# Optimization experiments

Hardware: AMD Instinct MI355X
Metric: run time of the kernel (lower is better)

The kernel has to match this reference:

```python
import jax, jax.numpy as jnp
import numpy as np

N, E = 50000, 800000
C, H, EC = 64, 3, 32  # node_channels, heads, edge_channels
NEG_SLOPE = 0.2


def _kaiming(key, shape, fan_in):
    bound = np.sqrt(6.0 / fan_in)  # kaiming_uniform_ default (a=sqrt(5)-ish approx; gain sqrt(2) variant)
    return jax.random.uniform(key, shape, jnp.float32, -bound, bound)


def setup_inputs() -> dict:
    key = jax.random.key(0)
    ks = jax.random.split(key, 8)
    x = jax.random.normal(ks[0], (N, C), jnp.float32)
    edge_index = jax.random.randint(ks[1], (2, E), 0, N, jnp.int64)
    edge_attr = jax.random.normal(ks[2], (E, EC), jnp.float32)
    weight_node = _kaiming(ks[3], (C, H * C), C)
    weight_edge = _kaiming(ks[4], (EC, H * C), EC)
    weight_triplet_att = _kaiming(ks[5], (1, H, 3 * C), 3 * C)
    weight_scale = _kaiming(ks[6], (H * C, C), H * C)
    bias = jnp.zeros((C,), jnp.float32)
    return {"x": x, "edge_index": edge_index, "edge_attr": edge_attr,
            "weight_node": weight_node, "weight_edge": weight_edge,
            "weight_triplet_att": weight_triplet_att,
            "weight_scale": weight_scale, "bias": bias}


def reference(x, edge_index, edge_attr, weight_node, weight_edge,
              weight_triplet_att, weight_scale, bias):
    src = edge_index[0]  # j (source)
    dst = edge_index[1]  # i (target), PyG default flow source_to_target

    xp = x @ weight_node                     # [N, H*C]
    ep = edge_attr @ weight_edge             # [E, H*C]

    x_j = xp[src].reshape(E, H, C)
    x_i = xp[dst].reshape(E, H, C)
    e_ij = ep.reshape(E, H, C)

    # attention weight split along concat order [x_i, e_ij, x_j]
    w = weight_triplet_att.reshape(H, 3, C)
    alpha = (jnp.einsum('ehc,hc->eh', x_i, w[:, 0])
             + jnp.einsum('ehc,hc->eh', e_ij, w[:, 1])
             + jnp.einsum('ehc,hc->eh', x_j, w[:, 2]))   # [E, H]
    alpha = jnp.where(alpha >= 0, alpha, NEG_SLOPE * alpha)  # leaky_relu

    # segment softmax over destination nodes (PyG softmax semantics)
    seg_max = jax.ops.segment_max(alpha, dst, num_segments=N)    # [N, H]
    alpha = jnp.exp(alpha - seg_max[dst])
    seg_sum = jax.ops.segment_sum(alpha, dst, num_segments=N)    # [N, H]
    alpha = alpha / (seg_sum[dst] + 1e-16)

    msg = alpha[:, :, None] * e_ij * x_j                         # [E, H, C]
    aggr = jax.ops.segment_sum(msg.reshape(E, H * C), dst, num_segments=N)  # [N, H*C]

    return aggr @ weight_scale + bias                            # [N, C]
```

## Files before the change

kernel.cpp:

```cpp
#include <hip/hip_runtime.h>

#define CC    64
#define HH    3
#define ECC   32
#define HCdim 192
#define NEG_SLOPE 0.2f
#define ASHIFT 12.0f
#define LOG2E  1.44269504f

typedef float v2f __attribute__((ext_vector_type(2)));
typedef _Float16 h2 __attribute__((ext_vector_type(2)));
typedef _Float16 h8 __attribute__((ext_vector_type(8)));

#if defined(__has_builtin)
#  if __has_builtin(__builtin_amdgcn_fdot2)
#    define USE_FDOT2 1
#  endif
#endif
#ifndef USE_FDOT2
#  define USE_FDOT2 0
#endif

#define K1_ROWS 64
__global__ __launch_bounds__(192) void tm_k1(const float* __restrict__ x,
        const float* __restrict__ Wn, const float* __restrict__ wt,
        const int* __restrict__ ei, int* __restrict__ deg,
        _Float16* __restrict__ xp16, float* __restrict__ sA, int N, int E) {
    __shared__ float wl[CC * HCdim];
    __shared__ float xl[K1_ROWS * CC];
    const int t = threadIdx.x;
    for (int i = blockIdx.x * 192 + t; i < E; i += gridDim.x * 192)
        atomicAdd(&deg[ei[E + i]], 1);
    const int h = t >> 6, c = t & 63;
    {
        float4* wl4 = (float4*)wl;
        const float4* Wn4 = (const float4*)Wn;
        for (int i = t; i < CC * HCdim / 4; i += 192) wl4[i] = Wn4[i];
    }
    const int base = blockIdx.x * K1_ROWS;
    const int rows = min(K1_ROWS, N - base);
    {
        float4* xl4 = (float4*)xl;
        const float4* x4 = (const float4*)(x + (size_t)base * CC);
        for (int i = t; i < rows * CC / 4; i += 192) xl4[i] = x4[i];
    }
    const float w0c = wt[h * HCdim + c];
    const float w2c = wt[h * HCdim + 2 * CC + c];
    __syncthreads();
    for (int rt = 0; rt < rows; rt += 4) {
        float acc0 = 0.f, acc1 = 0.f, acc2 = 0.f, acc3 = 0.f;
        #pragma unroll 4
        for (int k = 0; k < CC; k += 4) {
            const float w0  = wl[(k + 0) * HCdim + t];
            const float w1  = wl[(k + 1) * HCdim + t];
            const float w2_ = wl[(k + 2) * HCdim + t];
            const float w3  = wl[(k + 3) * HCdim + t];
            const float4 xa = *(const float4*)&xl[(rt + 0) * CC + k];
            const float4 xb = *(const float4*)&xl[(rt + 1) * CC + k];
            const float4 xc = *(const float4*)&xl[(rt + 2) * CC + k];
            const float4 xd = *(const float4*)&xl[(rt + 3) * CC + k];
            acc0 = fmaf(xa.x, w0, fmaf(xa.y, w1, fmaf(xa.z, w2_, fmaf(xa.w, w3, acc0))));
            acc1 = fmaf(xb.x, w0, fmaf(xb.y, w1, fmaf(xb.z, w2_, fmaf(xb.w, w3, acc1))));
            acc2 = fmaf(xc.x, w0, fmaf(xc.y, w1, fmaf(xc.z, w2_, fmaf(xc.w, w3, acc2))));
            acc3 = fmaf(xd.x, w0, fmaf(xd.y, w1, fmaf(xd.z, w2_, fmaf(xd.w, w3, acc3))));
        }
        #pragma unroll
        for (int r = 0; r < 4; ++r) {
            const float v = (r == 0) ? acc0 : (r == 1) ? acc1 : (r == 2) ? acc2 : acc3;
            const int n = base + rt + r;
            xp16[(size_t)n * HCdim + t] = (_Float16)v;
            float a0 = v * w0c, a2 = v * w2c;
            #pragma unroll
            for (int o = 32; o; o >>= 1) {
                a0 += __shfl_xor(a0, o);
                a2 += __shfl_xor(a2, o);
            }
            if (c == 0) {
                sA[n * 8 + h]     = a0;
                sA[n * 8 + 4 + h] = a2;
            }
        }
    }
}

__global__ __launch_bounds__(256) void tm_scanA(const int* __restrict__ deg,
        int* __restrict__ bsum, int N) {
    __shared__ int sd[256];
    int t = threadIdx.x, n = blockIdx.x * 256 + t;
    sd[t] = (n < N) ? deg[n] : 0;
    __syncthreads();
    for (int o = 128; o; o >>= 1) {
        if (t < o) sd[t] += sd[t + o];
        __syncthreads();
    }
    if (!t) bsum[blockIdx.x] = sd[0];
}

__global__ __launch_bounds__(256) void tm_scanC(const int* __restrict__ deg,
        const int* __restrict__ bsum, int* __restrict__ off,
        int* __restrict__ cursor, int N) {
    __shared__ int sd[256];
    __shared__ int pref;
    const int t = threadIdx.x, bid = blockIdx.x;
    const int n = bid * 256 + t;
    sd[t] = (t < bid) ? bsum[t] : 0;
    __syncthreads();
    for (int o = 128; o; o >>= 1) {
        if (t < o) sd[t] += sd[t + o];
        __syncthreads();
    }
    if (!t) pref = sd[0];
    __syncthreads();
    int v = (n < N) ? deg[n] : 0;
    sd[t] = v;
    __syncthreads();
    for (int o = 1; o < 256; o <<= 1) {
        int x = (t >= o) ? sd[t - o] : 0;
        __syncthreads();
        sd[t] += x;
        __syncthreads();
    }
    if (n < N) {
        int ex = pref + sd[t] - v;
        off[n] = ex;
        cursor[n] = ex;
        if (n == N - 1) off[N] = ex + v;
    }
}

__global__ __launch_bounds__(256) void tm_alpha(const int* __restrict__ ei,
        const float* __restrict__ ea, const float* __restrict__ We,
        const float* __restrict__ wt, const float* __restrict__ sA,
        int* __restrict__ cursor, float4* __restrict__ alphaE,
        int2* __restrict__ perm, _Float16* __restrict__ ea16, int E) {
    __shared__ float ul[HH * ECC];
    const int t = threadIdx.x;
    if (t < HH * ECC) {
        const int h = t >> 5, k = t & 31;
        float s = 0.f;
        #pragma unroll
        for (int c = 0; c < CC; ++c)
            s = fmaf(We[k * HCdim + h * CC + c], wt[h * HCdim + CC + c], s);
        ul[t] = s;
    }
    __syncthreads();
    const int e = blockIdx.x * 256 + t;
    if (e >= E) return;
    const int src = ei[e];
    const int dst = ei[E + e];
    float av[ECC];
    const float4* p4 = (const float4*)(ea + (size_t)e * ECC);
    #pragma unroll
    for (int q = 0; q < 8; ++q) {
        float4 v = p4[q];
        av[4*q] = v.x; av[4*q+1] = v.y; av[4*q+2] = v.z; av[4*q+3] = v.w;
    }
#if USE_FDOT2
    {
        h8* dst16 = (h8*)(ea16 + (size_t)e * ECC);
        #pragma unroll
        for (int b = 0; b < 4; ++b) {
            h8 o16;
            #pragma unroll
            for (int j = 0; j < 8; ++j) o16[j] = (_Float16)av[b * 8 + j];
            dst16[b] = o16;
        }
    }
#else
    (void)ea16;
#endif
    float d0 = 0.f, d1 = 0.f, d2 = 0.f;
    #pragma unroll
    for (int k = 0; k < ECC; ++k) {
        d0 = fmaf(av[k], ul[k], d0);
        d1 = fmaf(av[k], ul[ECC + k], d1);
        d2 = fmaf(av[k], ul[2 * ECC + k], d2);
    }
    const float4 s0 = *(const float4*)(sA + (size_t)dst * 8);
    const float4 s2 = *(const float4*)(sA + (size_t)src * 8 + 4);
    float a0 = s0.x + d0 + s2.x;
    float a1 = s0.y + d1 + s2.y;
    float a2 = s0.z + d2 + s2.z;
    a0 = (a0 >= 0.f) ? a0 : NEG_SLOPE * a0;
    a1 = (a1 >= 0.f) ? a1 : NEG_SLOPE * a1;
    a2 = (a2 >= 0.f) ? a2 : NEG_SLOPE * a2;
    alphaE[e] = make_float4(exp2f((a0 - ASHIFT) * LOG2E),
                            exp2f((a1 - ASHIFT) * LOG2E),
                            exp2f((a2 - ASHIFT) * LOG2E), 0.f);
    const int pos = atomicAdd(&cursor[dst], 1);
    perm[pos] = make_int2(src * (HCdim * 2), e * (ECC * 4));
}

__global__ __launch_bounds__(192) void tm_agg(const int2* __restrict__ perm,
        const int* __restrict__ off, const float* __restrict__ ea,
        const float* __restrict__ We, const float* __restrict__ alphaE,
        const _Float16* __restrict__ xp16, const _Float16* __restrict__ ea16,
        float* __restrict__ aggrN, int N) {
    const int t = threadIdx.x;
    const int h = t >> 6, lane = t & 63;
    const char* __restrict__ xp_b = (const char*)xp16;
    const char* __restrict__ al_b = (const char*)alphaE;
#if USE_FDOT2
    const char* __restrict__ e16_b = (const char*)ea16;
    h2 wc[16];
    #pragma unroll
    for (int k2 = 0; k2 < 16; ++k2) {
        h2 w;
        w[0] = (_Float16)We[(2 * k2)     * HCdim + h * CC + lane];
        w[1] = (_Float16)We[(2 * k2 + 1) * HCdim + h * CC + lane];
        wc[k2] = w;
    }
#else
    const char* __restrict__ ea_b = (const char*)ea;
    (void)ea16;
    v2f wcol2[16];
    #pragma unroll
    for (int k2 = 0; k2 < 16; ++k2) {
        wcol2[k2].x = We[(2 * k2)     * HCdim + h * CC + lane];
        wcol2[k2].y = We[(2 * k2 + 1) * HCdim + h * CC + lane];
    }
#endif
    const int xoff = h * (CC * 2) + lane * 2;
    const int aoff = h * 4;
    for (int n = blockIdx.x; n < N; n += gridDim.x) {
        const int start = off[n], end = off[n + 1];
        float s = 0.f, acc = 0.f;
        int pos = start;
        int4 pp = (pos + 2 <= end) ? *(const int4*)&perm[pos]
                                   : make_int4(0, 0, 0, 0);
        for (; pos + 2 <= end; ) {
            const int4 cur = pp;
            pos += 2;
            if (pos + 2 <= end) pp = *(const int4*)&perm[pos];
            const int so0 = __builtin_amdgcn_readfirstlane(cur.x);
            const int eo0 = __builtin_amdgcn_readfirstlane(cur.y);
            const int so1 = __builtin_amdgcn_readfirstlane(cur.z);
            const int eo1 = __builtin_amdgcn_readfirstlane(cur.w);
            const float p0 = *(const float*)(al_b + (eo0 >> 3) + aoff);
            const float p1 = *(const float*)(al_b + (eo1 >> 3) + aoff);
            const float xj0 = (float)*(const _Float16*)(xp_b + so0 + xoff);
            const float xj1 = (float)*(const _Float16*)(xp_b + so1 + xoff);
            float ep0, ep1;
#if USE_FDOT2
            const uint4 a0 = *(const uint4*)(e16_b + (eo0 >> 1));
            const uint4 a1 = *(const uint4*)(e16_b + (eo0 >> 1) + 16);
            const uint4 b0 = *(const uint4*)(e16_b + (eo1 >> 1));
            const uint4 b1 = *(const uint4*)(e16_b + (eo1 >> 1) + 16);
            float d0 = 0.f, d1 = 0.f;
            d0 = __builtin_amdgcn_fdot2(__builtin_bit_cast(h2, a0.x), wc[0], d0, false);
            d0 = __builtin_amdgcn_fdot2(__builtin_bit_cast(h2, a0.y), wc[1], d0, false);
            d0 = __builtin_amdgcn_fdot2(__builtin_bit_cast(h2, a0.z), wc[2], d0, false);
            d0 = __builtin_amdgcn_fdot2(__builtin_bit_cast(h2, a0.w), wc[3], d0, false);
            d0 = __builtin_amdgcn_fdot2(__builtin_bit_cast(h2, a1.x), wc[4], d0, false);
            d0 = __builtin_amdgcn_fdot2(__builtin_bit_cast(h2, a1.y), wc[5], d0, false);
            d0 = __builtin_amdgcn_fdot2(__builtin_bit_cast(h2, a1.z), wc[6], d0, false);
            d0 = __builtin_amdgcn_fdot2(__builtin_bit_cast(h2, a1.w), wc[7], d0, false);
            const uint4 a2 = *(const uint4*)(e16_b + (eo0 >> 1) + 32);
            const uint4 a3 = *(const uint4*)(e16_b + (eo0 >> 1) + 48);
            d0 = __builtin_amdgcn_fdot2(__builtin_bit_cast(h2, a2.x), wc[8],  d0, false);
            d0 = __builtin_amdgcn_fdot2(__builtin_bit_cast(h2, a2.y), wc[9],  d0, false);
            d0 = __builtin_amdgcn_fdot2(__builtin_bit_cast(h2, a2.z), wc[10], d0, false);
            d0 = __builtin_amdgcn_fdot2(__builtin_bit_cast(h2, a2.w), wc[11], d0, false);
            d0 = __builtin_amdgcn_fdot2(__builtin_bit_cast(h2, a3.x), wc[12], d0, false);
            d0 = __builtin_amdgcn_fdot2(__builtin_bit_cast(h2, a3.y), wc[13], d0, false);
            d0 = __builtin_amdgcn_fdot2(__builtin_bit_cast(h2, a3.z), wc[14], d0, false);
            d0 = __builtin_amdgcn_fdot2(__builtin_bit_cast(h2, a3.w), wc[15], d0, false);
            const uint4 b2 = *(const uint4*)(e16_b + (eo1 >> 1) + 32);
            const uint4 b3 = *(const uint4*)(e16_b + (eo1 >> 1) + 48);
            d1 = __builtin_amdgcn_fdot2(__builtin_bit_cast(h2, b0.x), wc[0],  d1, false);
            d1 = __builtin_amdgcn_fdot2(__builtin_bit_cast(h2, b0.y), wc[1],  d1, false);
            d1 = __builtin_amdgcn_fdot2(__builtin_bit_cast(h2, b0.z), wc[2],  d1, false);
            d1 = __builtin_amdgcn_fdot2(__builtin_bit_cast(h2, b0.w), wc[3],  d1, false);
            d1 = __builtin_amdgcn_fdot2(__builtin_bit_cast(h2, b1.x), wc[4],  d1, false);
            d1 = __builtin_amdgcn_fdot2(__builtin_bit_cast(h2, b1.y), wc[5],  d1, false);
            d1 = __builtin_amdgcn_fdot2(__builtin_bit_cast(h2, b1.z), wc[6],  d1, false);
            d1 = __builtin_amdgcn_fdot2(__builtin_bit_cast(h2, b1.w), wc[7],  d1, false);
            d1 = __builtin_amdgcn_fdot2(__builtin_bit_cast(h2, b2.x), wc[8],  d1, false);
            d1 = __builtin_amdgcn_fdot2(__builtin_bit_cast(h2, b2.y), wc[9],  d1, false);
            d1 = __builtin_amdgcn_fdot2(__builtin_bit_cast(h2, b2.z), wc[10], d1, false);
            d1 = __builtin_amdgcn_fdot2(__builtin_bit_cast(h2, b2.w), wc[11], d1, false);
            d1 = __builtin_amdgcn_fdot2(__builtin_bit_cast(h2, b3.x), wc[12], d1, false);
            d1 = __builtin_amdgcn_fdot2(__builtin_bit_cast(h2, b3.y), wc[13], d1, false);
            d1 = __builtin_amdgcn_fdot2(__builtin_bit_cast(h2, b3.z), wc[14], d1, false);
            d1 = __builtin_amdgcn_fdot2(__builtin_bit_cast(h2, b3.w), wc[15], d1, false);
            ep0 = d0; ep1 = d1;
#else
            const float4* q0 = (const float4*)(ea_b + eo0);
            const float4* q1 = (const float4*)(ea_b + eo1);
            v2f d0 = {0.f, 0.f}, d1 = {0.f, 0.f};
            #pragma unroll
            for (int q = 0; q < 8; ++q) {
                const float4 v0 = q0[q];
                const float4 v1 = q1[q];
                const v2f wlo = wcol2[2 * q], whi = wcol2[2 * q + 1];
                d0 = (v2f){v0.x, v0.y} * wlo + d0;
                d0 = (v2f){v0.z, v0.w} * whi + d0;
                d1 = (v2f){v1.x, v1.y} * wlo + d1;
                d1 = (v2f){v1.z, v1.w} * whi + d1;
            }
            ep0 = d0.x + d0.y; ep1 = d1.x + d1.y;
#endif
            s += p0 + p1;
            acc = fmaf(p0 * ep0, xj0, acc);
            acc = fmaf(p1 * ep1, xj1, acc);
        }
        if (pos < end) {
            const int2 pe = perm[pos];
            const int so = __builtin_amdgcn_readfirstlane(pe.x);
            const int eo = __builtin_amdgcn_readfirstlane(pe.y);
            const float p = *(const float*)(al_b + (eo >> 3) + aoff);
            const float xj = (float)*(const _Float16*)(xp_b + so + xoff);
            float ep;
#if USE_FDOT2
            const uint4 a0 = *(const uint4*)(e16_b + (eo >> 1));
            const uint4 a1 = *(const uint4*)(e16_b + (eo >> 1) + 16);
            const uint4 a2 = *(const uint4*)(e16_b + (eo >> 1) + 32);
            const uint4 a3 = *(const uint4*)(e16_b + (eo >> 1) + 48);
            float d = 0.f;
            d = __builtin_amdgcn_fdot2(__builtin_bit_cast(h2, a0.x), wc[0],  d, false);
            d = __builtin_amdgcn_fdot2(__builtin_bit_cast(h2, a0.y), wc[1],  d, false);
            d = __builtin_amdgcn_fdot2(__builtin_bit_cast(h2, a0.z), wc[2],  d, false);
            d = __builtin_amdgcn_fdot2(__builtin_bit_cast(h2, a0.w), wc[3],  d, false);
            d = __builtin_amdgcn_fdot2(__builtin_bit_cast(h2, a1.x), wc[4],  d, false);
            d = __builtin_amdgcn_fdot2(__builtin_bit_cast(h2, a1.y), wc[5],  d, false);
            d = __builtin_amdgcn_fdot2(__builtin_bit_cast(h2, a1.z), wc[6],  d, false);
            d = __builtin_amdgcn_fdot2(__builtin_bit_cast(h2, a1.w), wc[7],  d, false);
            d = __builtin_amdgcn_fdot2(__builtin_bit_cast(h2, a2.x), wc[8],  d, false);
            d = __builtin_amdgcn_fdot2(__builtin_bit_cast(h2, a2.y), wc[9],  d, false);
            d = __builtin_amdgcn_fdot2(__builtin_bit_cast(h2, a2.z), wc[10], d, false);
            d = __builtin_amdgcn_fdot2(__builtin_bit_cast(h2, a2.w), wc[11], d, false);
            d = __builtin_amdgcn_fdot2(__builtin_bit_cast(h2, a3.x), wc[12], d, false);
            d = __builtin_amdgcn_fdot2(__builtin_bit_cast(h2, a3.y), wc[13], d, false);
            d = __builtin_amdgcn_fdot2(__builtin_bit_cast(h2, a3.z), wc[14], d, false);
            d = __builtin_amdgcn_fdot2(__builtin_bit_cast(h2, a3.w), wc[15], d, false);
            ep = d;
#else
            const float4* q4 = (const float4*)(ea_b + eo);
            v2f d = {0.f, 0.f};
            #pragma unroll
            for (int q = 0; q < 8; ++q) {
                const float4 v = q4[q];
                d = (v2f){v.x, v.y} * wcol2[2 * q]     + d;
                d = (v2f){v.z, v.w} * wcol2[2 * q + 1] + d;
            }
            ep = d.x + d.y;
#endif
            s += p;
            acc = fmaf(p * ep, xj, acc);
        }
        aggrN[(size_t)n * HCdim + h * CC + lane] = acc / (s + 1e-16f);
    }
}

#define K5_ROWS 16
__global__ __launch_bounds__(256) void tm_k5(const float* __restrict__ aggrN,
        const float* __restrict__ Ws, const float* __restrict__ bias,
        float* __restrict__ out, int N) {
    __shared__ float wsl[HCdim * CC];
    __shared__ float al[K5_ROWS * HCdim];
    const int t = threadIdx.x;
    const int part = t >> 6, c = t & 63;
    {
        float4* w4 = (float4*)wsl;
        const float4* Ws4 = (const float4*)Ws;
        for (int i = t; i < HCdim * CC / 4; i += 256) w4[i] = Ws4[i];
    }
    const float b = bias[c];
    for (int base = blockIdx.x * K5_ROWS; base < N; base += gridDim.x * K5_ROWS) {
        const int rows = min(K5_ROWS, N - base);
        __syncthreads();
        {
            float4* al4 = (float4*)al;
            const float4* a4 = (const float4*)(aggrN + (size_t)base * HCdim);
            for (int i = t; i < rows * HCdim / 4; i += 256) al4[i] = a4[i];
        }
        __syncthreads();
        const int r0 = part * 4;
        if (r0 >= rows) continue;
        float acc0 = b, acc1 = b, acc2 = b, acc3 = b;
        #pragma unroll 4
        for (int k = 0; k < HCdim; k += 4) {
            const float w0  = wsl[(k + 0) * CC + c];
            const float w1  = wsl[(k + 1) * CC + c];
            const float w2_ = wsl[(k + 2) * CC + c];
            const float w3  = wsl[(k + 3) * CC + c];
            const float4 xa = *(const float4*)&al[(r0 + 0) * HCdim + k];
            const float4 xb = *(const float4*)&al[(r0 + 1) * HCdim + k];
            const float4 xc = *(const float4*)&al[(r0 + 2) * HCdim + k];
            const float4 xd = *(const float4*)&al[(r0 + 3) * HCdim + k];
            acc0 = fmaf(xa.x, w0, fmaf(xa.y, w1, fmaf(xa.z, w2_, fmaf(xa.w, w3, acc0))));
            acc1 = fmaf(xb.x, w0, fmaf(xb.y, w1, fmaf(xb.z, w2_, fmaf(xb.w, w3, acc1))));
            acc2 = fmaf(xc.x, w0, fmaf(xc.y, w1, fmaf(xc.z, w2_, fmaf(xc.w, w3, acc2))));
            acc3 = fmaf(xd.x, w0, fmaf(xd.y, w1, fmaf(xd.z, w2_, fmaf(xd.w, w3, acc3))));
        }
        if (r0 + 0 < rows) out[(size_t)(base + r0 + 0) * CC + c] = acc0;
        if (r0 + 1 < rows) out[(size_t)(base + r0 + 1) * CC + c] = acc1;
        if (r0 + 2 < rows) out[(size_t)(base + r0 + 2) * CC + c] = acc2;
        if (r0 + 3 < rows) out[(size_t)(base + r0 + 3) * CC + c] = acc3;
    }
}

extern "C" void kernel_launch(void* const* d_in, const int* in_sizes, int n_in,
                              void* d_out, int out_size, void* d_ws, size_t ws_size,
                              hipStream_t stream) {
    const float* x    = (const float*)d_in[0];
    const int*   ei   = (const int*)d_in[1];
    const float* ea   = (const float*)d_in[2];
    const float* Wn   = (const float*)d_in[3];
    const float* We   = (const float*)d_in[4];
    const float* wt   = (const float*)d_in[5];
    const float* Ws   = (const float*)d_in[6];
    const float* bias = (const float*)d_in[7];
    float* out = (float*)d_out;
    const int N = in_sizes[0] / CC;
    const int E = in_sizes[1] / 2;
    const int nb = (N + 255) / 256;

    float* ws = (float*)d_ws;
    size_t o = 0;
    _Float16* xp16 = (_Float16*)(ws + o); o += (size_t)N * HCdim / 2;
    float* sA = ws + o;                  o += (size_t)N * 8;
    float4* alphaE = (float4*)(ws + o);  o += (size_t)E * 4;
    int2*  perm = (int2*)(ws + o);       o += (size_t)E * 2 + 32;
    _Float16* ea16 = (_Float16*)(ws + o); o += (size_t)E * ECC / 2;
    int* deg    = (int*)(ws + o);        o += N;
    int* off    = (int*)(ws + o);        o += N + 1;
    int* cursor = (int*)(ws + o);        o += N;
    int* bsum   = (int*)(ws + o);        o += 256;
    o += (4 - (o & 3)) & 3;
    float* aggrN = ws + o;               o += (size_t)N * HCdim;
    (void)ws_size; (void)n_in; (void)out_size;

    (void)hipMemsetAsync(deg, 0, (size_t)N * sizeof(int), stream);

    tm_k1<<<(N + K1_ROWS - 1) / K1_ROWS, 192, 0, stream>>>(x, Wn, wt, ei, deg,
                                                           xp16, sA, N, E);
    tm_scanA<<<nb, 256, 0, stream>>>(deg, bsum, N);
    tm_scanC<<<nb, 256, 0, stream>>>(deg, bsum, off, cursor, N);
    tm_alpha<<<(E + 255) / 256, 256, 0, stream>>>(ei, ea, We, wt, sA, cursor,
                                                  alphaE, perm, ea16, E);
    tm_agg<<<(N + 7) / 8, 192, 0, stream>>>(perm, off, ea, We,
                                            (const float*)alphaE, xp16, ea16,
                                            aggrN, N);
    tm_k5<<<512, 256, 0, stream>>>(aggrN, Ws, bias, out, N);
}
```

Measured before the change: 390.1 us.

## Write edge data in destination-sorted order to make aggregation reads contiguous

The alpha kernel now writes each edge's exp-alpha values and source offset as one int4 record, and its fp16 edge attributes, at the edge's CSR position rather than its original index. The aggregation kernel then reads records and edge features sequentially per destination node instead of through an indirection, which removes the perm lookup and the random gathers of alpha and edge features. In exchange the scattered writes in the alpha kernel grow to 64 bytes of features per edge at random positions, and the prefetch of the next perm pair is gone.

```diff
diff --git a/kernel.cpp b/kernel.cpp
--- a/kernel.cpp
+++ b/kernel.cpp
@@ -131,8 +131,8 @@
 __global__ __launch_bounds__(256) void tm_alpha(const int* __restrict__ ei,
         const float* __restrict__ ea, const float* __restrict__ We,
         const float* __restrict__ wt, const float* __restrict__ sA,
-        int* __restrict__ cursor, float4* __restrict__ alphaE,
-        int2* __restrict__ perm, _Float16* __restrict__ ea16, int E) {
+        int* __restrict__ cursor, int4* __restrict__ rec,
+        _Float16* __restrict__ ea16P, int E) {
     __shared__ float ul[HH * ECC];
     const int t = threadIdx.x;
     if (t < HH * ECC) {
@@ -155,20 +155,6 @@
         float4 v = p4[q];
         av[4*q] = v.x; av[4*q+1] = v.y; av[4*q+2] = v.z; av[4*q+3] = v.w;
     }
-#if USE_FDOT2
-    {
-        h8* dst16 = (h8*)(ea16 + (size_t)e * ECC);
-        #pragma unroll
-        for (int b = 0; b < 4; ++b) {
-            h8 o16;
-            #pragma unroll
-            for (int j = 0; j < 8; ++j) o16[j] = (_Float16)av[b * 8 + j];
-            dst16[b] = o16;
-        }
-    }
-#else
-    (void)ea16;
-#endif
     float d0 = 0.f, d1 = 0.f, d2 = 0.f;
     #pragma unroll
     for (int k = 0; k < ECC; ++k) {
@@ -184,24 +170,37 @@
     a0 = (a0 >= 0.f) ? a0 : NEG_SLOPE * a0;
     a1 = (a1 >= 0.f) ? a1 : NEG_SLOPE * a1;
     a2 = (a2 >= 0.f) ? a2 : NEG_SLOPE * a2;
-    alphaE[e] = make_float4(exp2f((a0 - ASHIFT) * LOG2E),
-                            exp2f((a1 - ASHIFT) * LOG2E),
-                            exp2f((a2 - ASHIFT) * LOG2E), 0.f);
+    const float p0 = exp2f((a0 - ASHIFT) * LOG2E);
+    const float p1 = exp2f((a1 - ASHIFT) * LOG2E);
+    const float p2 = exp2f((a2 - ASHIFT) * LOG2E);
     const int pos = atomicAdd(&cursor[dst], 1);
-    perm[pos] = make_int2(src * (HCdim * 2), e * (ECC * 4));
-}
-
-__global__ __launch_bounds__(192) void tm_agg(const int2* __restrict__ perm,
-        const int* __restrict__ off, const float* __restrict__ ea,
-        const float* __restrict__ We, const float* __restrict__ alphaE,
-        const _Float16* __restrict__ xp16, const _Float16* __restrict__ ea16,
+    int4 r;
+    r.x = src * (HCdim * 2);
+    r.y = __builtin_bit_cast(int, p0);
+    r.z = __builtin_bit_cast(int, p1);
+    r.w = __builtin_bit_cast(int, p2);
+    rec[pos] = r;
+    {
+        h8* dst16 = (h8*)(ea16P + (size_t)pos * ECC);
+        #pragma unroll
+        for (int b = 0; b < 4; ++b) {
+            h8 o16;
+            #pragma unroll
+            for (int j = 0; j < 8; ++j) o16[j] = (_Float16)av[b * 8 + j];
+            dst16[b] = o16;
+        }
+    }
+}
+
+__global__ __launch_bounds__(192) void tm_agg(const int4* __restrict__ rec,
+        const int* __restrict__ off, const float* __restrict__ We,
+        const _Float16* __restrict__ xp16, const _Float16* __restrict__ ea16P,
         float* __restrict__ aggrN, int N) {
     const int t = threadIdx.x;
     const int h = t >> 6, lane = t & 63;
     const char* __restrict__ xp_b = (const char*)xp16;
-    const char* __restrict__ al_b = (const char*)alphaE;
+    const char* __restrict__ ep_b = (const char*)ea16P;
 #if USE_FDOT2
-    const char* __restrict__ e16_b = (const char*)ea16;
     h2 wc[16];
     #pragma unroll
     for (int k2 = 0; k2 < 16; ++k2) {
@@ -211,8 +210,6 @@
         wc[k2] = w;
     }
 #else
-    const char* __restrict__ ea_b = (const char*)ea;
-    (void)ea16;
     v2f wcol2[16];
     #pragma unroll
     for (int k2 = 0; k2 < 16; ++k2) {
@@ -221,42 +218,35 @@
     }
 #endif
     const int xoff = h * (CC * 2) + lane * 2;
-    const int aoff = h * 4;
     for (int n = blockIdx.x; n < N; n += gridDim.x) {
         const int start = off[n], end = off[n + 1];
         float s = 0.f, acc = 0.f;
         int pos = start;
-        int4 pp = (pos + 2 <= end) ? *(const int4*)&perm[pos]
-                                   : make_int4(0, 0, 0, 0);
-        for (; pos + 2 <= end; ) {
-            const int4 cur = pp;
-            pos += 2;
-            if (pos + 2 <= end) pp = *(const int4*)&perm[pos];
-            const int so0 = __builtin_amdgcn_readfirstlane(cur.x);
-            const int eo0 = __builtin_amdgcn_readfirstlane(cur.y);
-            const int so1 = __builtin_amdgcn_readfirstlane(cur.z);
-            const int eo1 = __builtin_amdgcn_readfirstlane(cur.w);
-            const float p0 = *(const float*)(al_b + (eo0 >> 3) + aoff);
-            const float p1 = *(const float*)(al_b + (eo1 >> 3) + aoff);
+        for (; pos + 2 <= end; pos += 2) {
+            const int4 r0 = rec[pos];
+            const int4 r1 = rec[pos + 1];
+            const int so0 = __builtin_amdgcn_readfirstlane(r0.x);
+            const int so1 = __builtin_amdgcn_readfirstlane(r1.x);
+            const float p0 = __builtin_bit_cast(float,
+                __builtin_amdgcn_readfirstlane(h == 0 ? r0.y : h == 1 ? r0.z : r0.w));
+            const float p1 = __builtin_bit_cast(float,
+                __builtin_amdgcn_readfirstlane(h == 0 ? r1.y : h == 1 ? r1.z : r1.w));
             const float xj0 = (float)*(const _Float16*)(xp_b + so0 + xoff);
             const float xj1 = (float)*(const _Float16*)(xp_b + so1 + xoff);
+            const uint4* q = (const uint4*)(ep_b + ((size_t)pos << 6));
             float ep0, ep1;
 #if USE_FDOT2
-            const uint4 a0 = *(const uint4*)(e16_b + (eo0 >> 1));
-            const uint4 a1 = *(const uint4*)(e16_b + (eo0 >> 1) + 16);
-            const uint4 b0 = *(const uint4*)(e16_b + (eo1 >> 1));
-            const uint4 b1 = *(const uint4*)(e16_b + (eo1 >> 1) + 16);
+            const uint4 a0 = q[0], a1 = q[1], a2 = q[2], a3 = q[3];
+            const uint4 b0 = q[4], b1 = q[5], b2 = q[6], b3 = q[7];
             float d0 = 0.f, d1 = 0.f;
-            d0 = __builtin_amdgcn_fdot2(__builtin_bit_cast(h2, a0.x), wc[0], d0, false);
-            d0 = __builtin_amdgcn_fdot2(__builtin_bit_cast(h2, a0.y), wc[1], d0, false);
-            d0 = __builtin_amdgcn_fdot2(__builtin_bit_cast(h2, a0.z), wc[2], d0, false);
-            d0 = __builtin_amdgcn_fdot2(__builtin_bit_cast(h2, a0.w), wc[3], d0, false);
-            d0 = __builtin_amdgcn_fdot2(__builtin_bit_cast(h2, a1.x), wc[4], d0, false);
-            d0 = __builtin_amdgcn_fdot2(__builtin_bit_cast(h2, a1.y), wc[5], d0, false);
-            d0 = __builtin_amdgcn_fdot2(__builtin_bit_cast(h2, a1.z), wc[6], d0, false);
-            d0 = __builtin_amdgcn_fdot2(__builtin_bit_cast(h2, a1.w), wc[7], d0, false);
-            const uint4 a2 = *(const uint4*)(e16_b + (eo0 >> 1) + 32);
-            const uint4 a3 = *(const uint4*)(e16_b + (eo0 >> 1) + 48);
+            d0 = __builtin_amdgcn_fdot2(__builtin_bit_cast(h2, a0.x), wc[0],  d0, false);
+            d0 = __builtin_amdgcn_fdot2(__builtin_bit_cast(h2, a0.y), wc[1],  d0, false);
+            d0 = __builtin_amdgcn_fdot2(__builtin_bit_cast(h2, a0.z), wc[2],  d0, false);
+            d0 = __builtin_amdgcn_fdot2(__builtin_bit_cast(h2, a0.w), wc[3],  d0, false);
+            d0 = __builtin_amdgcn_fdot2(__builtin_bit_cast(h2, a1.x), wc[4],  d0, false);
+            d0 = __builtin_amdgcn_fdot2(__builtin_bit_cast(h2, a1.y), wc[5],  d0, false);
+            d0 = __builtin_amdgcn_fdot2(__builtin_bit_cast(h2, a1.z), wc[6],  d0, false);
+            d0 = __builtin_amdgcn_fdot2(__builtin_bit_cast(h2, a1.w), wc[7],  d0, false);
             d0 = __builtin_amdgcn_fdot2(__builtin_bit_cast(h2, a2.x), wc[8],  d0, false);
             d0 = __builtin_amdgcn_fdot2(__builtin_bit_cast(h2, a2.y), wc[9],  d0, false);
             d0 = __builtin_amdgcn_fdot2(__builtin_bit_cast(h2, a2.z), wc[10], d0, false);
@@ -265,8 +255,6 @@
             d0 = __builtin_amdgcn_fdot2(__builtin_bit_cast(h2, a3.y), wc[13], d0, false);
             d0 = __builtin_amdgcn_fdot2(__builtin_bit_cast(h2, a3.z), wc[14], d0, false);
             d0 = __builtin_amdgcn_fdot2(__builtin_bit_cast(h2, a3.w), wc[15], d0, false);
-            const uint4 b2 = *(const uint4*)(e16_b + (eo1 >> 1) + 32);
-            const uint4 b3 = *(const uint4*)(e16_b + (eo1 >> 1) + 48);
             d1 = __builtin_amdgcn_fdot2(__builtin_bit_cast(h2, b0.x), wc[0],  d1, false);
             d1 = __builtin_amdgcn_fdot2(__builtin_bit_cast(h2, b0.y), wc[1],  d1, false);
             d1 = __builtin_amdgcn_fdot2(__builtin_bit_cast(h2, b0.z), wc[2],  d1, false);
@@ -285,37 +273,32 @@
             d1 = __builtin_amdgcn_fdot2(__builtin_bit_cast(h2, b3.w), wc[15], d1, false);
             ep0 = d0; ep1 = d1;
 #else
-            const float4* q0 = (const float4*)(ea_b + eo0);
-            const float4* q1 = (const float4*)(ea_b + eo1);
+            const h2* e0 = (const h2*)(ep_b + ((size_t)pos << 6));
+            const h2* e1 = (const h2*)(ep_b + ((size_t)(pos + 1) << 6));
             v2f d0 = {0.f, 0.f}, d1 = {0.f, 0.f};
             #pragma unroll
-            for (int q = 0; q < 8; ++q) {
-                const float4 v0 = q0[q];
-                const float4 v1 = q1[q];
-                const v2f wlo = wcol2[2 * q], whi = wcol2[2 * q + 1];
-                d0 = (v2f){v0.x, v0.y} * wlo + d0;
-                d0 = (v2f){v0.z, v0.w} * whi + d0;
-                d1 = (v2f){v1.x, v1.y} * wlo + d1;
-                d1 = (v2f){v1.z, v1.w} * whi + d1;
+            for (int k2 = 0; k2 < 16; ++k2) {
+                const h2 u0 = e0[k2], u1 = e1[k2];
+                d0 = (v2f){(float)u0[0], (float)u0[1]} * wcol2[k2] + d0;
+                d1 = (v2f){(float)u1[0], (float)u1[1]} * wcol2[k2] + d1;
             }
             ep0 = d0.x + d0.y; ep1 = d1.x + d1.y;
+            (void)q;
 #endif
             s += p0 + p1;
             acc = fmaf(p0 * ep0, xj0, acc);
             acc = fmaf(p1 * ep1, xj1, acc);
         }
         if (pos < end) {
-            const int2 pe = perm[pos];
-            const int so = __builtin_amdgcn_readfirstlane(pe.x);
-            const int eo = __builtin_amdgcn_readfirstlane(pe.y);
-            const float p = *(const float*)(al_b + (eo >> 3) + aoff);
+            const int4 r0 = rec[pos];
+            const int so = __builtin_amdgcn_readfirstlane(r0.x);
+            const float p = __builtin_bit_cast(float,
+                __builtin_amdgcn_readfirstlane(h == 0 ? r0.y : h == 1 ? r0.z : r0.w));
             const float xj = (float)*(const _Float16*)(xp_b + so + xoff);
             float ep;
 #if USE_FDOT2
-            const uint4 a0 = *(const uint4*)(e16_b + (eo >> 1));
-            const uint4 a1 = *(const uint4*)(e16_b + (eo >> 1) + 16);
-            const uint4 a2 = *(const uint4*)(e16_b + (eo >> 1) + 32);
-            const uint4 a3 = *(const uint4*)(e16_b + (eo >> 1) + 48);
+            const uint4* q = (const uint4*)(ep_b + ((size_t)pos << 6));
+            const uint4 a0 = q[0], a1 = q[1], a2 = q[2], a3 = q[3];
             float d = 0.f;
             d = __builtin_amdgcn_fdot2(__builtin_bit_cast(h2, a0.x), wc[0],  d, false);
             d = __builtin_amdgcn_fdot2(__builtin_bit_cast(h2, a0.y), wc[1],  d, false);
@@ -335,13 +318,12 @@
             d = __builtin_amdgcn_fdot2(__builtin_bit_cast(h2, a3.w), wc[15], d, false);
             ep = d;
 #else
-            const float4* q4 = (const float4*)(ea_b + eo);
+            const h2* e0 = (const h2*)(ep_b + ((size_t)pos << 6));
             v2f d = {0.f, 0.f};
             #pragma unroll
-            for (int q = 0; q < 8; ++q) {
-                const float4 v = q4[q];
-                d = (v2f){v.x, v.y} * wcol2[2 * q]     + d;
-                d = (v2f){v.z, v.w} * wcol2[2 * q + 1] + d;
+            for (int k2 = 0; k2 < 16; ++k2) {
+                const h2 u0 = e0[k2];
+                d = (v2f){(float)u0[0], (float)u0[1]} * wcol2[k2] + d;
             }
             ep = d.x + d.y;
 #endif
@@ -420,9 +402,9 @@
     size_t o = 0;
     _Float16* xp16 = (_Float16*)(ws + o); o += (size_t)N * HCdim / 2;
     float* sA = ws + o;                  o += (size_t)N * 8;
-    float4* alphaE = (float4*)(ws + o);  o += (size_t)E * 4;
-    int2*  perm = (int2*)(ws + o);       o += (size_t)E * 2 + 32;
-    _Float16* ea16 = (_Float16*)(ws + o); o += (size_t)E * ECC / 2;
+    o += (16 - (o & 15)) & 15;
+    int4* rec = (int4*)(ws + o);         o += (size_t)E * 4;
+    _Float16* ea16P = (_Float16*)(ws + o); o += (size_t)E * ECC / 2;
     int* deg    = (int*)(ws + o);        o += N;
     int* off    = (int*)(ws + o);        o += N + 1;
     int* cursor = (int*)(ws + o);        o += N;
@@ -438,9 +420,7 @@
     tm_scanA<<<nb, 256, 0, stream>>>(deg, bsum, N);
     tm_scanC<<<nb, 256, 0, stream>>>(deg, bsum, off, cursor, N);
     tm_alpha<<<(E + 255) / 256, 256, 0, stream>>>(ei, ea, We, wt, sA, cursor,
-                                                  alphaE, perm, ea16, E);
-    tm_agg<<<(N + 7) / 8, 192, 0, stream>>>(perm, off, ea, We,
-                                            (const float*)alphaE, xp16, ea16,
-                                            aggrN, N);
+                                                  rec, ea16P, E);
+    tm_agg<<<(N + 7) / 8, 192, 0, stream>>>(rec, off, We, xp16, ea16P, aggrN, N);
     tm_k5<<<512, 256, 0, stream>>>(aggrN, Ws, bias, out, N);
 }
```

Result: slower. 416.4 us (+6.7%).
